# Optimization experiments

Measured on AMD Instinct MI355X. Metric: run time of the kernel, lower is better.

The kernel has to match this reference:

```python
import jax, jax.numpy as jnp
import numpy as np

N_NODES = 100000
N_EDGES = 3200000
F_IN = 128
F_OUT = 16


def setup_inputs() -> dict:
    key = jax.random.key(0)
    k1, k2, k3, k4, k5 = jax.random.split(key, 5)
    x = jax.random.normal(k1, (N_NODES, F_IN), dtype=jnp.float32)
    edge_index = jax.random.randint(k2, (2, N_EDGES), 0, N_NODES, dtype=jnp.int64)
    edge_weights = jax.random.uniform(k3, (N_EDGES,), dtype=jnp.float32)
    W = jax.random.normal(k4, (F_IN, F_OUT), dtype=jnp.float32) / np.sqrt(F_IN)
    b = jax.random.normal(k5, (F_OUT,), dtype=jnp.float32)
    return {"x": x, "edge_index": edge_index, "edge_weights": edge_weights, "W": W, "b": b}


def reference(x, edge_index, edge_weights, W, b):
    # GCNConv: out = D^{-1/2} (A + I) D^{-1/2} X W + b  (weighted edges, self-loops)
    n = x.shape[0]
    row = edge_index[0]  # source nodes
    col = edge_index[1]  # target nodes (aggregation destination)
    # add self-loops with weight 1.0 (GCNConv default)
    loop = jnp.arange(n, dtype=row.dtype)
    row_f = jnp.concatenate([row, loop])
    col_f = jnp.concatenate([col, loop])
    ew = jnp.concatenate([edge_weights, jnp.ones((n,), dtype=edge_weights.dtype)])
    # symmetric normalization: deg over destination, norm = d^{-1/2}[row] * w * d^{-1/2}[col]
    deg = jax.ops.segment_sum(ew, col_f, num_segments=n)
    dinv = jnp.where(deg > 0, jax.lax.rsqrt(deg), 0.0)
    norm = dinv[row_f] * ew * dinv[col_f]  # [E+N]
    h = x @ W  # [N, F_OUT] dense projection before propagation
    msgs = h[row_f] * norm[:, None]  # gather + scale, [E+N, F_OUT]
    out = jax.ops.segment_sum(msgs, col_f, num_segments=n)  # scatter-add
    return out + b
```

## Files before the change

kernel.cpp:

```cpp
#include <hip/hip_runtime.h>

#define N_NODES 100000
#define N_EDGES 3200000
#define F_IN 128
#define F_OUT 16

#define NSEG 512
#define EPS (N_EDGES / NSEG)
#define NBUCK 512
#define NPB 196
#define GEMM_BLOCKS ((N_NODES + 15) / 16)
#define MAXREC 7424
#define CLMASK 255

#define OFF_NCNT  0u
#define OFF_TOT   0x200000u
#define OFF_BASE  0x202000u
#define OFF_DINV  0x210000u
#define OFF_NPTR  0x280000u
#define OFF_HH    0x300000u
#define OFF_GG    0x920000u
#define OFF_TT    0x920000u
#define OFF_CSR   0x1000000u
#define WS_NEEDED ((size_t)0x1000000 + (size_t)N_EDGES * 8)

__device__ __forceinline__ unsigned short f2bf(float f) {
    unsigned u = __float_as_uint(f);
    unsigned r = (u + 0x7FFFu + ((u >> 16) & 1u)) >> 16;
    return (unsigned short)r;
}
__device__ __forceinline__ float bf2f(unsigned short v) {
    return __uint_as_float((unsigned)v << 16);
}


__global__ void k_hist_gemm(const int* __restrict__ col,
                            int* __restrict__ Tt,
                            const float* __restrict__ x,
                            const float* __restrict__ W,
                            float* __restrict__ h) {
    __shared__ int smem[2048];
    int tid = threadIdx.x;
    if (blockIdx.x < NSEG) {
        int s = blockIdx.x;
        for (int i = tid; i < NBUCK; i += 256) smem[i] = 0;
        __syncthreads();
        int e0 = s * EPS;
        for (int i = tid; i < EPS; i += 256)
            atomicAdd(&smem[col[e0 + i] / NPB], 1);
        __syncthreads();
        for (int i = tid; i < NBUCK; i += 256)
            Tt[(size_t)i * NSEG + s] = smem[i];
    } else {
        float* Ws = (float*)smem;
        for (int i = tid; i < F_IN * F_OUT; i += 256) Ws[i] = W[i];
        __syncthreads();
        int n = (blockIdx.x - NSEG) * 16 + (tid >> 4);
        int j = tid & 15;
        if (n >= N_NODES) return;
        const float4* xr = (const float4*)(x + (size_t)n * F_IN);
        float acc = 0.0f;
#pragma unroll
        for (int k4 = 0; k4 < F_IN / 4; ++k4) {
            float4 xv = xr[k4];
            int k = k4 * 4;
            acc += xv.x * Ws[(k + 0) * F_OUT + j];
            acc += xv.y * Ws[(k + 1) * F_OUT + j];
            acc += xv.z * Ws[(k + 2) * F_OUT + j];
            acc += xv.w * Ws[(k + 3) * F_OUT + j];
        }
        h[(size_t)n * F_OUT + j] = acc;
    }
}

__global__ void k_scan_a(int* __restrict__ Tt, int* __restrict__ tot) {
    int tid = threadIdx.x;
    int b = blockIdx.x * 4 + (tid >> 6);
    int l = tid & 63;
    int4* row = (int4*)Tt + (size_t)b * (NSEG / 4);
    int4 v0 = row[l];
    int4 v1 = row[l + 64];
    int s0 = v0.x + v0.y + v0.z + v0.w;
    int inc0 = s0;
    for (int off = 1; off < 64; off <<= 1) {
        int t = __shfl_up(inc0, off);
        if (l >= off) inc0 += t;
    }
    int exc0 = inc0 - s0;
    int tot0 = __shfl(inc0, 63);
    int s1 = v1.x + v1.y + v1.z + v1.w;
    int inc1 = s1;
    for (int off = 1; off < 64; off <<= 1) {
        int t = __shfl_up(inc1, off);
        if (l >= off) inc1 += t;
    }
    int exc1 = inc1 - s1 + tot0;
    int4 o0, o1;
    o0.x = exc0;
    o0.y = exc0 + v0.x;
    o0.z = o0.y + v0.y;
    o0.w = o0.z + v0.z;
    o1.x = exc1;
    o1.y = exc1 + v1.x;
    o1.z = o1.y + v1.y;
    o1.w = o1.z + v1.z;
    row[l] = o0;
    row[l + 64] = o1;
    if (l == 63) tot[b] = inc1 + tot0;
}

__global__ void k_scan_b(const int* __restrict__ tot, int* __restrict__ base) {
    __shared__ int s[256];
    int tid = threadIdx.x;
    const int4* t4 = (const int4*)tot;
    int4 p = (tid < NBUCK / 4) ? t4[tid] : make_int4(0, 0, 0, 0);
    int lsum = p.x + p.y + p.z + p.w;
    s[tid] = lsum;
    __syncthreads();
    for (int off = 1; off < 256; off <<= 1) {
        int t = (tid >= off) ? s[tid - off] : 0;
        __syncthreads();
        s[tid] += t;
        __syncthreads();
    }
    int run = s[tid] - lsum;
    if (tid < NBUCK / 4) {
        int4 o;
        o.x = run; run += p.x;
        o.y = run; run += p.y;
        o.z = run; run += p.z;
        o.w = run;
        ((int4*)base)[tid] = o;
    }
}

__global__ void __launch_bounds__(512) k_bin(const int* __restrict__ row,
                                             const int* __restrict__ col,
                                             const float* __restrict__ ew,
                                             const int* __restrict__ Tt,
                                             const int* __restrict__ base,
                                             int2* __restrict__ csr) {
    __shared__ int2 srec[EPS];
    __shared__ int lcnt[NBUCK];
    __shared__ int lpre[NBUCK + 1];
    __shared__ int gofs[NBUCK];
    int tid = threadIdx.x;
    int s = blockIdx.x;
    int e0 = s * EPS;

    lcnt[tid] = 0;
    __syncthreads();
    for (int i = tid; i < EPS; i += 512)
        atomicAdd(&lcnt[col[e0 + i] / NPB], 1);
    __syncthreads();

    int v = lcnt[tid];
    gofs[tid] = v;
    __syncthreads();
    for (int off = 1; off < 512; off <<= 1) {
        int t = (tid >= off) ? gofs[tid - off] : 0;
        __syncthreads();
        gofs[tid] += t;
        __syncthreads();
    }
    int excl = gofs[tid] - v;
    lpre[tid] = excl;
    if (tid == 0) lpre[NBUCK] = EPS;
    __syncthreads();
    gofs[tid] = base[tid] + Tt[(size_t)tid * NSEG + s] - excl;
    lcnt[tid] = excl;
    __syncthreads();

    for (int i = tid; i < EPS; i += 512) {
        int e = e0 + i;
        int r = row[e];
        int c = col[e];
        int bk = c / NPB;
        int pos = atomicAdd(&lcnt[bk], 1);
        int2 rec;
        rec.x = (r << 8) | (c - bk * NPB);
        rec.y = __float_as_int(ew[e]);
        srec[pos] = rec;
    }
    __syncthreads();

    for (int t = tid; t < EPS; t += 512) {
        int lo = 0, hi = NBUCK;
        while (hi - lo > 1) {
            int mid = (lo + hi) >> 1;
            if (lpre[mid] <= t) lo = mid; else hi = mid;
        }
        csr[gofs[lo] + t] = srec[t];
    }
}

__global__ void k_sort(const int* __restrict__ base,
                       const int* __restrict__ tot,
                       int2* __restrict__ csr,
                       const float* __restrict__ h,
                       float* __restrict__ dinv,
                       unsigned short* __restrict__ gb,
                       int* __restrict__ nodeptr,
                       int* __restrict__ ncnt) {
    __shared__ int2 srec[MAXREC];
    __shared__ int cnt[256];
    __shared__ float wsum[256];
    __shared__ int cur[256];
    __shared__ float dl[256];
    int tid = threadIdx.x;
    int b = blockIdx.x;
    int c0 = b * NPB;
    int bseg = base[b];
    int total = tot[b];
    bool ovf = (total > MAXREC);
    int nstage = ovf ? MAXREC : total;

    cnt[tid] = 0;
    wsum[tid] = 1.0f;
    __syncthreads();

    for (int i = tid; i < nstage; i += 256) {
        int2 rec = csr[bseg + i];
        srec[i] = rec;
        atomicAdd(&cnt[rec.x & CLMASK], 1);
        atomicAdd(&wsum[rec.x & CLMASK], __int_as_float(rec.y));
    }
    for (int i = nstage + tid; i < total; i += 256) {
        int2 rec = csr[bseg + i];
        atomicAdd(&cnt[rec.x & CLMASK], 1);
        atomicAdd(&wsum[rec.x & CLMASK], __int_as_float(rec.y));
    }
    __syncthreads();

    if (tid < 64) {
        int l = tid;
        int a0 = cnt[4 * l], a1 = cnt[4 * l + 1], a2 = cnt[4 * l + 2], a3 = cnt[4 * l + 3];
        int ssum = a0 + a1 + a2 + a3;
        int incl = ssum;
        for (int off = 1; off < 64; off <<= 1) {
            int t = __shfl_up(incl, off);
            if (l >= off) incl += t;
        }
        int run = incl - ssum;
        int av[4] = {a0, a1, a2, a3};
        for (int k = 0; k < 4; ++k) {
            int bin = 4 * l + k;
            cur[bin] = run;
            float d = rsqrtf(wsum[bin]);
            dl[bin] = d;
            int n = c0 + bin;
            if (bin < NPB && n < N_NODES) {
                dinv[n] = d;
                nodeptr[n] = ovf ? bseg : (bseg + run);
                ncnt[n] = ovf ? -total : av[k];
            }
            run += av[k];
        }
    }
    __syncthreads();

    if (!ovf) {
        for (int i = tid; i < total; i += 256) {
            int2 rec = srec[i];
            int pos = atomicAdd(&cur[rec.x & CLMASK], 1);
            int2 o;
            o.x = rec.x >> 8;
            o.y = rec.y;
            csr[bseg + pos] = o;
        }
    }

    for (int i = tid; i < NPB * F_OUT; i += 256) {
        int idx = c0 * F_OUT + i;
        if (idx < N_NODES * F_OUT) gb[idx] = f2bf(dl[i >> 4] * h[idx]);
    }
}

__global__ void k_pull2(const int* __restrict__ nodeptr,
                        const int* __restrict__ ncnt,
                        const int2* __restrict__ csr,
                        const unsigned short* __restrict__ gb,
                        const float* __restrict__ dinv,
                        const float* __restrict__ bias,
                        float* __restrict__ out) {
    int n = blockIdx.x * 4 + (threadIdx.x >> 6);
    if (n >= N_NODES) return;
    int lane = threadIdx.x & 63;
    int s = lane >> 4;
    int j = lane & 15;
    int p0 = nodeptr[n];
    int cnt = ncnt[n];
    float bj = bias[j];
    float acc = 0.0f;
    if (cnt >= 0) {
#pragma unroll 4
        for (int i = s; i < cnt; i += 4) {
            int2 rec = csr[p0 + i];
            acc += bf2f(gb[(size_t)rec.x * F_OUT + j]) * __int_as_float(rec.y);
        }
    } else {
        int total = -cnt;
        int cl = n - (n / NPB) * NPB;
        for (int i = s; i < total; i += 4) {
            int2 rec = csr[p0 + i];
            if ((rec.x & CLMASK) == cl)
                acc += bf2f(gb[(size_t)(rec.x >> 8) * F_OUT + j]) * __int_as_float(rec.y);
        }
    }
    acc += __shfl_xor(acc, 16);
    acc += __shfl_xor(acc, 32);
    if (s == 0) {
        float dn = dinv[n];
        float gs = bf2f(gb[(size_t)n * F_OUT + j]);
        out[(size_t)n * F_OUT + j] = bj + dn * (gs + acc);
    }
}


#define EDGE_BLOCKS_FB ((N_EDGES + 255) / 256)
__global__ void k_init_fb(float* __restrict__ deg) {
    int i = blockIdx.x * blockDim.x + threadIdx.x;
    if (i < N_NODES) deg[i] = 1.0f;
}
__global__ void k_fused_fb(const int* __restrict__ col, const float* __restrict__ ew,
                           float* __restrict__ deg, const float* __restrict__ x,
                           const float* __restrict__ W, float* __restrict__ h) {
    int b3 = blockIdx.x / 3;
    int r3 = blockIdx.x % 3;
    if (r3 < 2) {
        int e = (b3 * 2 + r3) * 256 + threadIdx.x;
        if (e < N_EDGES) atomicAdd(&deg[col[e]], ew[e]);
    } else {
        __shared__ float Ws[F_IN * F_OUT];
        int tid = threadIdx.x;
        for (int i = tid; i < F_IN * F_OUT; i += 256) Ws[i] = W[i];
        __syncthreads();
        int n = b3 * 16 + (tid >> 4);
        int j = tid & 15;
        if (n >= N_NODES) return;
        const float4* xr = (const float4*)(x + (size_t)n * F_IN);
        float acc = 0.0f;
#pragma unroll
        for (int k4 = 0; k4 < F_IN / 4; ++k4) {
            float4 xv = xr[k4];
            int k = k4 * 4;
            acc += xv.x * Ws[(k + 0) * F_OUT + j];
            acc += xv.y * Ws[(k + 1) * F_OUT + j];
            acc += xv.z * Ws[(k + 2) * F_OUT + j];
            acc += xv.w * Ws[(k + 3) * F_OUT + j];
        }
        h[(size_t)n * F_OUT + j] = acc;
    }
}
__global__ void k_final_fb(float* __restrict__ deg, const float* __restrict__ h,
                           const float* __restrict__ b, float* __restrict__ g,
                           float* __restrict__ out) {
    int i = blockIdx.x * blockDim.x + threadIdx.x;
    int n = i >> 4;
    int j = i & 15;
    if (n >= N_NODES) return;
    float d = rsqrtf(deg[n]);
    if (j == 0) deg[n] = d;
    float gg = d * h[i];
    g[i] = gg;
    out[i] = b[j] + d * gg;
}
__global__ void k_scatter_fb(const int* __restrict__ row, const int* __restrict__ col,
                             const float* __restrict__ ew, const float* __restrict__ dinv,
                             const float* __restrict__ g, float* __restrict__ out) {
    long long tid = (long long)blockIdx.x * blockDim.x + threadIdx.x;
    int e = (int)(tid >> 4);
    int j = (int)(tid & 15);
    if (e >= N_EDGES) return;
    int c = col[e];
    float norm = ew[e] * dinv[c];
    atomicAdd(&out[(size_t)c * F_OUT + j], g[(size_t)row[e] * F_OUT + j] * norm);
}

extern "C" void kernel_launch(void* const* d_in, const int* in_sizes, int n_in,
                              void* d_out, int out_size, void* d_ws, size_t ws_size,
                              hipStream_t stream) {
    const float* x  = (const float*)d_in[0];
    const int*   ei = (const int*)d_in[1];
    const float* ew = (const float*)d_in[2];
    const float* W  = (const float*)d_in[3];
    const float* b  = (const float*)d_in[4];
    float* out = (float*)d_out;

    const int* row = ei;
    const int* col = ei + N_EDGES;

    char* ws = (char*)d_ws;
    dim3 blk(256);

    if (ws_size >= WS_NEEDED) {
        int*   ncnt = (int*)(ws + OFF_NCNT);
        int*   tot  = (int*)(ws + OFF_TOT);
        int*   base = (int*)(ws + OFF_BASE);
        float* dinv = (float*)(ws + OFF_DINV);
        int*   nptr = (int*)(ws + OFF_NPTR);
        float* h    = (float*)(ws + OFF_HH);
        unsigned short* gb = (unsigned short*)(ws + OFF_GG);
        int*   Tt   = (int*)(ws + OFF_TT);
        int2*  csr  = (int2*)(ws + OFF_CSR);

        k_hist_gemm<<<NSEG + GEMM_BLOCKS, blk, 0, stream>>>(col, Tt, x, W, h);
        k_scan_a<<<NBUCK / 4, blk, 0, stream>>>(Tt, tot);
        k_scan_b<<<1, blk, 0, stream>>>(tot, base);
        k_bin<<<NSEG, 512, 0, stream>>>(row, col, ew, Tt, base, csr);
        k_sort<<<NBUCK, blk, 0, stream>>>(base, tot, csr, h, dinv, gb, nptr, ncnt);
        k_pull2<<<(N_NODES + 3) / 4, blk, 0, stream>>>(nptr, ncnt, csr, gb, dinv, b, out);
    } else {
        float* deg = (float*)ws;
        float* h   = (float*)(ws + (1u << 20));
        float* g   = (float*)(ws + (8u << 20));
        k_init_fb<<<(N_NODES + 255) / 256, blk, 0, stream>>>(deg);
        k_fused_fb<<<EDGE_BLOCKS_FB + GEMM_BLOCKS, blk, 0, stream>>>(col, ew, deg, x, W, h);
        k_final_fb<<<(N_NODES * F_OUT + 255) / 256, blk, 0, stream>>>(deg, h, b, g, out);
        long long total = (long long)N_EDGES * F_OUT;
        k_scatter_fb<<<(unsigned)((total + 255) / 256), blk, 0, stream>>>(row, col, ew, deg, g, out);
    }
}
```

Measured before the change: 268.6 us.

## Replace per-node sort and pull with bucket-level LDS atomic aggregation

Drops the intra-bucket counting sort and per-node CSR pull. Degree sums are now computed with global float atomics during the histogram pass, and a separate prep kernel builds dinv and the scaled bf16 features. A 1024-thread block per bucket then accumulates messages into shared memory with atomics before writing the output. This removes the sort's LDS staging, the second CSR rewrite and the overflow path, at the cost of 3.2M global float atomics and shared-memory atomic contention.

```diff
diff --git a/kernel.cpp b/kernel.cpp
--- a/kernel.cpp
+++ b/kernel.cpp
@@ -10,14 +10,12 @@
 #define NBUCK 512
 #define NPB 196
 #define GEMM_BLOCKS ((N_NODES + 15) / 16)
-#define MAXREC 7424
 #define CLMASK 255
 
-#define OFF_NCNT  0u
+#define OFF_WSUM  0u
 #define OFF_TOT   0x200000u
 #define OFF_BASE  0x202000u
 #define OFF_DINV  0x210000u
-#define OFF_NPTR  0x280000u
 #define OFF_HH    0x300000u
 #define OFF_GG    0x920000u
 #define OFF_TT    0x920000u
@@ -34,8 +32,15 @@
 }
 
 
+__global__ void k_init(float* __restrict__ wsum) {
+    int i = blockIdx.x * 256 + threadIdx.x;
+    if (i < N_NODES) wsum[i] = 1.0f;
+}
+
 __global__ void k_hist_gemm(const int* __restrict__ col,
+                            const float* __restrict__ ew,
                             int* __restrict__ Tt,
+                            float* __restrict__ wsum,
                             const float* __restrict__ x,
                             const float* __restrict__ W,
                             float* __restrict__ h) {
@@ -46,8 +51,11 @@
         for (int i = tid; i < NBUCK; i += 256) smem[i] = 0;
         __syncthreads();
         int e0 = s * EPS;
-        for (int i = tid; i < EPS; i += 256)
-            atomicAdd(&smem[col[e0 + i] / NPB], 1);
+        for (int i = tid; i < EPS; i += 256) {
+            int c = col[e0 + i];
+            atomicAdd(&smem[c / NPB], 1);
+            atomicAdd(&wsum[c], ew[e0 + i]);
+        }
         __syncthreads();
         for (int i = tid; i < NBUCK; i += 256)
             Tt[(size_t)i * NSEG + s] = smem[i];
@@ -194,125 +202,56 @@
     }
 }
 
-__global__ void k_sort(const int* __restrict__ base,
-                       const int* __restrict__ tot,
-                       int2* __restrict__ csr,
+__global__ void k_prep(const float* __restrict__ wsum,
                        const float* __restrict__ h,
                        float* __restrict__ dinv,
-                       unsigned short* __restrict__ gb,
-                       int* __restrict__ nodeptr,
-                       int* __restrict__ ncnt) {
-    __shared__ int2 srec[MAXREC];
-    __shared__ int cnt[256];
-    __shared__ float wsum[256];
-    __shared__ int cur[256];
-    __shared__ float dl[256];
+                       unsigned short* __restrict__ gb) {
+    int t = blockIdx.x * 256 + threadIdx.x;
+    if (t >= N_NODES * 4) return;
+    int n = t >> 2;
+    float d = rsqrtf(wsum[n]);
+    if ((t & 3) == 0) dinv[n] = d;
+    float4 hv = ((const float4*)h)[t];
+    unsigned o0 = (unsigned)f2bf(d * hv.x) | ((unsigned)f2bf(d * hv.y) << 16);
+    unsigned o1 = (unsigned)f2bf(d * hv.z) | ((unsigned)f2bf(d * hv.w) << 16);
+    uint2 o; o.x = o0; o.y = o1;
+    ((uint2*)gb)[t] = o;
+}
+
+__global__ void __launch_bounds__(1024) k_agg(const int* __restrict__ base,
+                                              const int* __restrict__ tot,
+                                              const int2* __restrict__ csr,
+                                              const unsigned short* __restrict__ gb,
+                                              const float* __restrict__ dinv,
+                                              const float* __restrict__ bias,
+                                              float* __restrict__ out) {
+    __shared__ float acc[NPB * F_OUT];
     int tid = threadIdx.x;
     int b = blockIdx.x;
     int c0 = b * NPB;
+    for (int i = tid; i < NPB * F_OUT; i += 1024) acc[i] = 0.0f;
+    __syncthreads();
+
     int bseg = base[b];
     int total = tot[b];
-    bool ovf = (total > MAXREC);
-    int nstage = ovf ? MAXREC : total;
-
-    cnt[tid] = 0;
-    wsum[tid] = 1.0f;
-    __syncthreads();
-
-    for (int i = tid; i < nstage; i += 256) {
+    int g16 = tid >> 4;
+    int j = tid & 15;
+#pragma unroll 4
+    for (int i = g16; i < total; i += 64) {
         int2 rec = csr[bseg + i];
-        srec[i] = rec;
-        atomicAdd(&cnt[rec.x & CLMASK], 1);
-        atomicAdd(&wsum[rec.x & CLMASK], __int_as_float(rec.y));
-    }
-    for (int i = nstage + tid; i < total; i += 256) {
-        int2 rec = csr[bseg + i];
-        atomicAdd(&cnt[rec.x & CLMASK], 1);
-        atomicAdd(&wsum[rec.x & CLMASK], __int_as_float(rec.y));
-    }
-    __syncthreads();
-
-    if (tid < 64) {
-        int l = tid;
-        int a0 = cnt[4 * l], a1 = cnt[4 * l + 1], a2 = cnt[4 * l + 2], a3 = cnt[4 * l + 3];
-        int ssum = a0 + a1 + a2 + a3;
-        int incl = ssum;
-        for (int off = 1; off < 64; off <<= 1) {
-            int t = __shfl_up(incl, off);
-            if (l >= off) incl += t;
-        }
-        int run = incl - ssum;
-        int av[4] = {a0, a1, a2, a3};
-        for (int k = 0; k < 4; ++k) {
-            int bin = 4 * l + k;
-            cur[bin] = run;
-            float d = rsqrtf(wsum[bin]);
-            dl[bin] = d;
-            int n = c0 + bin;
-            if (bin < NPB && n < N_NODES) {
-                dinv[n] = d;
-                nodeptr[n] = ovf ? bseg : (bseg + run);
-                ncnt[n] = ovf ? -total : av[k];
-            }
-            run += av[k];
-        }
-    }
-    __syncthreads();
-
-    if (!ovf) {
-        for (int i = tid; i < total; i += 256) {
-            int2 rec = srec[i];
-            int pos = atomicAdd(&cur[rec.x & CLMASK], 1);
-            int2 o;
-            o.x = rec.x >> 8;
-            o.y = rec.y;
-            csr[bseg + pos] = o;
-        }
-    }
-
-    for (int i = tid; i < NPB * F_OUT; i += 256) {
-        int idx = c0 * F_OUT + i;
-        if (idx < N_NODES * F_OUT) gb[idx] = f2bf(dl[i >> 4] * h[idx]);
-    }
-}
-
-__global__ void k_pull2(const int* __restrict__ nodeptr,
-                        const int* __restrict__ ncnt,
-                        const int2* __restrict__ csr,
-                        const unsigned short* __restrict__ gb,
-                        const float* __restrict__ dinv,
-                        const float* __restrict__ bias,
-                        float* __restrict__ out) {
-    int n = blockIdx.x * 4 + (threadIdx.x >> 6);
-    if (n >= N_NODES) return;
-    int lane = threadIdx.x & 63;
-    int s = lane >> 4;
-    int j = lane & 15;
-    int p0 = nodeptr[n];
-    int cnt = ncnt[n];
-    float bj = bias[j];
-    float acc = 0.0f;
-    if (cnt >= 0) {
-#pragma unroll 4
-        for (int i = s; i < cnt; i += 4) {
-            int2 rec = csr[p0 + i];
-            acc += bf2f(gb[(size_t)rec.x * F_OUT + j]) * __int_as_float(rec.y);
-        }
-    } else {
-        int total = -cnt;
-        int cl = n - (n / NPB) * NPB;
-        for (int i = s; i < total; i += 4) {
-            int2 rec = csr[p0 + i];
-            if ((rec.x & CLMASK) == cl)
-                acc += bf2f(gb[(size_t)(rec.x >> 8) * F_OUT + j]) * __int_as_float(rec.y);
-        }
-    }
-    acc += __shfl_xor(acc, 16);
-    acc += __shfl_xor(acc, 32);
-    if (s == 0) {
-        float dn = dinv[n];
-        float gs = bf2f(gb[(size_t)n * F_OUT + j]);
-        out[(size_t)n * F_OUT + j] = bj + dn * (gs + acc);
+        float v = bf2f(gb[(size_t)(rec.x >> 8) * F_OUT + j]) * __int_as_float(rec.y);
+        atomicAdd(&acc[(rec.x & CLMASK) * F_OUT + j], v);
+    }
+    __syncthreads();
+
+    for (int i = tid; i < NPB * F_OUT; i += 1024) {
+        int n = c0 + (i >> 4);
+        if (n < N_NODES) {
+            int jj = i & 15;
+            float d = dinv[n];
+            float gs = bf2f(gb[(size_t)n * F_OUT + jj]);
+            out[(size_t)n * F_OUT + jj] = bias[jj] + d * (gs + acc[i]);
+        }
     }
 }
 
@@ -394,22 +333,22 @@
     dim3 blk(256);
 
     if (ws_size >= WS_NEEDED) {
-        int*   ncnt = (int*)(ws + OFF_NCNT);
+        float* wsum = (float*)(ws + OFF_WSUM);
         int*   tot  = (int*)(ws + OFF_TOT);
         int*   base = (int*)(ws + OFF_BASE);
         float* dinv = (float*)(ws + OFF_DINV);
-        int*   nptr = (int*)(ws + OFF_NPTR);
         float* h    = (float*)(ws + OFF_HH);
         unsigned short* gb = (unsigned short*)(ws + OFF_GG);
         int*   Tt   = (int*)(ws + OFF_TT);
         int2*  csr  = (int2*)(ws + OFF_CSR);
 
-        k_hist_gemm<<<NSEG + GEMM_BLOCKS, blk, 0, stream>>>(col, Tt, x, W, h);
+        k_init<<<(N_NODES + 255) / 256, blk, 0, stream>>>(wsum);
+        k_hist_gemm<<<NSEG + GEMM_BLOCKS, blk, 0, stream>>>(col, ew, Tt, wsum, x, W, h);
         k_scan_a<<<NBUCK / 4, blk, 0, stream>>>(Tt, tot);
         k_scan_b<<<1, blk, 0, stream>>>(tot, base);
         k_bin<<<NSEG, 512, 0, stream>>>(row, col, ew, Tt, base, csr);
-        k_sort<<<NBUCK, blk, 0, stream>>>(base, tot, csr, h, dinv, gb, nptr, ncnt);
-        k_pull2<<<(N_NODES + 3) / 4, blk, 0, stream>>>(nptr, ncnt, csr, gb, dinv, b, out);
+        k_prep<<<(N_NODES * 4 + 255) / 256, blk, 0, stream>>>(wsum, h, dinv, gb);
+        k_agg<<<NBUCK, 1024, 0, stream>>>(base, tot, csr, gb, dinv, b, out);
     } else {
         float* deg = (float*)ws;
         float* h   = (float*)(ws + (1u << 20));
```

Measured after the change: 582.9 us. +117.0%, slower.
